# Kernel optimization log

Measured on AMD Instinct MI355X. Metric: run time of the kernel, lower is better.

Reference implementation:

```python
import jax, jax.numpy as jnp
import numpy as np

# dims
B, L, HID = 4, 4096, 1024
H, D = 16, 64            # num_mem_heads, head_dim = HID // H
DM = 128                 # mem_intermediate = head_dim * mem_expansion_factor (2.0)
K = 4                    # conv_kernel
CS = 64                  # chunk_size
EPS = 1e-6


def setup_inputs() -> dict:
    key = jax.random.key(0)
    ks = jax.random.split(key, 16)
    std = 0.02
    f = lambda i, shape: jax.random.normal(ks[i], shape, jnp.float32) * std
    return {
        'hidden_states': jax.random.normal(ks[0], (B, L, HID), jnp.float32),
        'Wq': f(1, (HID, HID)), 'Wk': f(2, (HID, HID)), 'Wv': f(3, (HID, HID)),
        'conv_q_w': f(4, (HID, K)), 'conv_q_b': jnp.zeros((HID,), jnp.float32),
        'conv_k_w': f(5, (HID, K)), 'conv_k_b': jnp.zeros((HID,), jnp.float32),
        'conv_v_w': f(6, (HID, K)), 'conv_v_b': jnp.zeros((HID,), jnp.float32),
        'q_norm_w': jnp.ones((D,), jnp.float32), 'k_norm_w': jnp.ones((D,), jnp.float32),
        'mem_decay_w': f(7, (H, HID)), 'mem_decay_b': jnp.zeros((H,), jnp.float32),
        'surprise_w': f(8, (H, HID)), 'surprise_b': jnp.zeros((H,), jnp.float32),
        'lr_w': f(9, (H, HID)), 'lr_b': jnp.zeros((H,), jnp.float32),
        'W1': f(10, (H, D, DM)), 'W2': f(11, (H, DM, D)),
    }


def _silu_bwd(x):
    sig = jax.nn.sigmoid(x)
    return sig + jax.nn.silu(x) * (1.0 - sig)


def _rmsnorm(x, w):
    xf = x.astype(jnp.float32)
    var = jnp.mean(xf * xf, axis=-1, keepdims=True)
    return w * (xf * jax.lax.rsqrt(var + EPS)).astype(x.dtype)


def _causal_conv_silu(x, w, b):
    # x: [B, L, H, D] -> depthwise causal conv over time on C=H*D channels -> [B, H, L, D]
    Bs, Ls, Hh, Dd = x.shape
    xc = jnp.swapaxes(x.reshape(Bs, Ls, Hh * Dd), 1, 2)        # [B, C, L]
    xp = jnp.pad(xc, ((0, 0), (0, 0), (K - 1, 0)))             # left pad -> causal
    y = b[None, :, None]
    for k in range(K):
        y = y + w[None, :, k:k + 1] * xp[:, :, k:k + Ls]
    y = jax.nn.silu(y)
    return jnp.swapaxes(y.reshape(Bs, Hh, Dd, Ls), -2, -1)     # [B, H, L, D]


def _decayed_scan(d, v, init):
    # y_t = d_t * y_{t-1} + v_t, y_0 = init; d: [B,H,C,1], v: [B,H,C,dim], init: [B,H,1,dim]
    def comb(x, y):
        a1, b1 = x
        a2, b2 = y
        return a1 * a2, b1 * a2 + b2
    A, Bv = jax.lax.associative_scan(comb, (d, v), axis=2)
    return A * init + Bv


def _forward(hidden_states, Wq, Wk, Wv, conv_q_w, conv_q_b, conv_k_w, conv_k_b,
             conv_v_w, conv_v_b, q_norm_w, k_norm_w, mem_decay_w, mem_decay_b,
             surprise_w, surprise_b, lr_w, lr_b, W1, W2):
    x = hidden_states
    # projections -> [B, L, H, D]
    q = (x @ Wq.T).reshape(B, L, H, D)
    k = (x @ Wk.T).reshape(B, L, H, D)
    v = (x @ Wv.T).reshape(B, L, H, D)
    # depthwise causal conv + silu -> [B, H, L, D]
    q = _causal_conv_silu(q, conv_q_w, conv_q_b)
    k = _causal_conv_silu(k, conv_k_w, conv_k_b)
    v = _causal_conv_silu(v, conv_v_w, conv_v_b)
    # QK RMSNorm (per head_dim)
    q = _rmsnorm(q, q_norm_w)
    k = _rmsnorm(k, k_norm_w)
    # per-timestep gates -> [B, H, L, 1]
    mem_decay = 1.0 - jax.nn.sigmoid(x @ mem_decay_w.T + mem_decay_b)
    surprise_decay = jax.nn.sigmoid(x @ surprise_w.T + surprise_b)
    lr = jax.nn.sigmoid(x @ lr_w.T + lr_b)
    to_gate = lambda g: jnp.swapaxes(g, -2, -1)[..., None]
    mem_decay, surprise_decay, lr = to_gate(mem_decay), to_gate(surprise_decay), to_gate(lr)

    # split sequence into chunks: [N, B, H, CS, *]
    N = L // CS
    ch = lambda t: jnp.moveaxis(t.reshape(B, H, N, CS, t.shape[-1]), 2, 0)
    qs, ks_, vs = ch(q), ch(k), ch(v)
    mds, sds, lrs = ch(mem_decay), ch(surprise_decay), ch(lr)

    W1b = jnp.broadcast_to(W1[None], (B, H, D, DM))
    W2b = jnp.broadcast_to(W2[None], (B, H, DM, D))
    carry0 = (W1b, W2b,
              jnp.zeros((B, H, 1, DM), jnp.float32),   # W1_surprise
              jnp.zeros((B, H, 1, D), jnp.float32),    # W2_surprise
              jnp.zeros((B, H, 1, D), jnp.float32),    # key_momentum
              jnp.zeros((B, H, 1, DM), jnp.float32))   # X1_momentum

    def step(carry, inp):
        W1c, W2c, W1s, W2s, kmom, xmom = carry
        qc, kc, vc, md, sd, lrc = inp
        # memory MLP fwd with chunk-frozen weights
        Z1 = kc @ W1c                       # [B,H,CS,DM]
        X1 = jax.nn.silu(Z1)
        mems = X1 @ W2c                     # [B,H,CS,D]
        g_m = mems - vc
        g_Z1 = (g_m @ jnp.swapaxes(W2c, -2, -1)) * _silu_bwd(Z1)
        g_m = -lrc * g_m
        g_Z1 = -lrc * g_Z1
        # activation-space surprise/momentum scans (decayed linear recurrence)
        W1s_n = _decayed_scan(sd, g_Z1, W1s)[:, :, -1:, :]
        W2s_n = _decayed_scan(sd, g_m, W2s)[:, :, -1:, :]
        kmom_n = _decayed_scan(md, kc, kmom)[:, :, -1:, :]
        xmom_n = _decayed_scan(md, X1, xmom)[:, :, -1:, :]
        # weight update at chunk boundary: decay + outer-product of accumulated factors
        mprod = jnp.prod(md, axis=2, keepdims=True)          # [B,H,1,1]
        W1n = mprod * W1c + jnp.swapaxes(kmom_n, -2, -1) @ W1s_n
        W2n = mprod * W2c + jnp.swapaxes(xmom_n, -2, -1) @ W2s_n
        # retrieve with updated memory
        y = jax.nn.silu(qc @ W1n) @ W2n                      # [B,H,CS,D]
        return (W1n, W2n, W1s_n, W2s_n, kmom_n, xmom_n), y

    _, ys = jax.lax.scan(step, carry0, (qs, ks_, vs, mds, sds, lrs))
    mem_states = jnp.moveaxis(ys, 0, 2).reshape(B, H, L, D)
    # replicate torch: mem_states.transpose(-2,-1).reshape(B, L, H*D)
    return jnp.swapaxes(mem_states, -2, -1).reshape(B, L, H * D)


def reference(hidden_states, Wq, Wk, Wv, conv_q_w, conv_q_b, conv_k_w, conv_k_b,
              conv_v_w, conv_v_b, q_norm_w, k_norm_w, mem_decay_w, mem_decay_b,
              surprise_w, surprise_b, lr_w, lr_b, W1, W2):
    return _forward(hidden_states, Wq, Wk, Wv, conv_q_w, conv_q_b, conv_k_w, conv_k_b,
                    conv_v_w, conv_v_b, q_norm_w, k_norm_w, mem_decay_w, mem_decay_b,
                    surprise_w, surprise_b, lr_w, lr_b, W1, W2)
```

## Files before the change

### kernel.cpp

```cpp
#include <hip/hip_runtime.h>

#define B_ 4
#define L_ 4096
#define HID_ 1024
#define H_ 16
#define D_ 64
#define DM_ 128
#define CS_ 64
#define NCH_ 64
#define EPS_ 1e-6f

typedef __attribute__((ext_vector_type(8))) short bfrag_t;
typedef __attribute__((ext_vector_type(4))) float facc_t;

#define MFMA16(a,b,c) __builtin_amdgcn_mfma_f32_16x16x32_bf16(a,b,c,0,0,0)

__device__ __forceinline__ float sigf(float x){ return 1.0f/(1.0f + __expf(-x)); }

__device__ __forceinline__ unsigned f2bfu(float x){
  unsigned u = __float_as_uint(x);
  return (u + 0x7fffu + ((u>>16)&1u)) >> 16;
}
__device__ __forceinline__ float bf2f(unsigned short s){
  return __uint_as_float(((unsigned)s)<<16);
}
__device__ __forceinline__ unsigned cvtpk(float lo, float hi){
  unsigned r;
  asm("v_cvt_pk_bf16_f32 %0, %1, %2" : "=v"(r) : "v"(lo), "v"(hi));
  return r;
}
__device__ __forceinline__ float bflo(unsigned u){ return __uint_as_float(u<<16); }
__device__ __forceinline__ float bfhi(unsigned u){ return __uint_as_float(u & 0xffff0000u); }

__device__ __forceinline__ void gld16(const unsigned short* g, unsigned short* l){
  __builtin_amdgcn_global_load_lds(
      (const __attribute__((address_space(1))) unsigned int*)(const void*)g,
      (__attribute__((address_space(3))) unsigned int*)(void*)l,
      16, 0, 0);
}

#define DPP_ADD_(x, ctrl) x += __int_as_float(__builtin_amdgcn_update_dpp(0, __float_as_int(x), ctrl, 0xf, 0xf, true))
__device__ __forceinline__ float wsum64(float x){
  DPP_ADD_(x, 0x111);
  DPP_ADD_(x, 0x112);
  DPP_ADD_(x, 0x114);
  DPP_ADD_(x, 0x118);
  const float a = __int_as_float(__builtin_amdgcn_readlane(__float_as_int(x), 15));
  const float b = __int_as_float(__builtin_amdgcn_readlane(__float_as_int(x), 31));
  const float c = __int_as_float(__builtin_amdgcn_readlane(__float_as_int(x), 47));
  const float d = __int_as_float(__builtin_amdgcn_readlane(__float_as_int(x), 63));
  return (a+b)+(c+d);
}

__global__ __launch_bounds__(256) void cast_kernel(
    const float* __restrict__ x,  const float* __restrict__ wq,
    const float* __restrict__ wk, const float* __restrict__ wv,
    unsigned short* __restrict__ xb,  unsigned short* __restrict__ wqb,
    unsigned short* __restrict__ wkb, unsigned short* __restrict__ wvb)
{
  const int bid = blockIdx.x;
  const float* s; unsigned short* d; int base;
  if (bid < 16384){ s = x; d = xb; base = bid*1024; }
  else {
    int r = bid - 16384; const int a = r >> 10; r &= 1023; base = r*1024;
    s = (a==0)?wq:(a==1)?wk:wv;
    d = (a==0)?wqb:(a==1)?wkb:wvb;
  }
  const int i = base + threadIdx.x*4;
  float4 v = *(const float4*)(s + i);
  unsigned lo = f2bfu(v.x) | (f2bfu(v.y)<<16);
  unsigned hi = f2bfu(v.z) | (f2bfu(v.w)<<16);
  uint2 o; o.x = lo; o.y = hi;
  *(uint2*)(d + i) = o;
}

__global__ __launch_bounds__(256, 2) void gemm_bf16_nt(
    const unsigned short* __restrict__ A, const unsigned short* __restrict__ Bw,
    unsigned short* __restrict__ C, int M, int N, int K)
{
  __shared__ __align__(16) unsigned short As[2][4096];
  __shared__ __align__(16) unsigned short Bs[2][4096];
  const int tid = threadIdx.x;
  const int lane = tid & 63, wave = tid >> 6;
  const int lq = lane & 15, quad = lane >> 4;
  const int m0 = blockIdx.y*128, n0 = blockIdx.x*128;
  const int row = tid >> 2, ks = (tid & 3)*8;
  const int mo = (wave & 1)*64, no = (wave >> 1)*64;

  const unsigned short* pa0 = A  + (size_t)(m0 + row)*K + ks;
  const unsigned short* pa1 = pa0 + (size_t)64*K;
  const unsigned short* pb0 = Bw + (size_t)(n0 + row)*K + ks;
  const unsigned short* pb1 = pb0 + (size_t)64*K;

  facc_t acc[4][4];
  #pragma unroll
  for (int i=0;i<4;++i)
    #pragma unroll
    for (int j=0;j<4;++j) acc[i][j] = (facc_t){0.f,0.f,0.f,0.f};

  auto stage = [&](int buf, int kt){
    const int off = kt*32;
    unsigned short* ab = &As[buf][wave*512];
    unsigned short* bb = &Bs[buf][wave*512];
    gld16(pa0 + off, ab);
    gld16(pa1 + off, ab + 2048);
    gld16(pb0 + off, bb);
    gld16(pb1 + off, bb + 2048);
  };

  const int kiters = K >> 5;
  stage(0, 0);
  __syncthreads();

  int cur = 0;
  for (int kt = 0; kt < kiters; ++kt){
    if (kt+1 < kiters) stage(cur^1, kt+1);
    bfrag_t af[4], bf[4];
    #pragma unroll
    for (int mt=0;mt<4;++mt) af[mt] = *(const bfrag_t*)&As[cur][(mo+mt*16+lq)*32 + quad*8];
    #pragma unroll
    for (int nt=0;nt<4;++nt) bf[nt] = *(const bfrag_t*)&Bs[cur][(no+nt*16+lq)*32 + quad*8];
    #pragma unroll
    for (int mt=0;mt<4;++mt)
      #pragma unroll
      for (int nt=0;nt<4;++nt)
        acc[mt][nt] = MFMA16(af[mt], bf[nt], acc[mt][nt]);
    __syncthreads();
    cur ^= 1;
  }

  #pragma unroll
  for (int mt=0;mt<4;++mt)
    #pragma unroll
    for (int nt=0;nt<4;++nt)
      #pragma unroll
      for (int r=0;r<4;++r){
        const int rr = m0 + mo + mt*16 + quad*4 + r;
        const int cc = n0 + no + nt*16 + lq;
        const int t = cc >> 10, hh = (cc >> 6) & 15, dd = cc & 63;
        const int b = rr >> 12, l = rr & 4095;
        C[((((size_t)t*B_ + b)*H_ + hh)*L_ + l)*64 + dd]
            = (unsigned short)f2bfu(acc[mt][nt][r]);
      }
}

__global__ __launch_bounds__(256, 2) void gates_kernel(
  const float* __restrict__ x,
  const float* __restrict__ mdw, const float* __restrict__ mdb,
  const float* __restrict__ sw,  const float* __restrict__ sb,
  const float* __restrict__ lw,  const float* __restrict__ lb,
  float* __restrict__ cmb, float* __restrict__ c1b, float* __restrict__ ppb)
{
  __shared__ float xs[64][68];
  __shared__ float wg[48][68];
  const int tid = threadIdx.x;
  const int m0 = blockIdx.x * 64;
  const int tx = tid & 15, ty = tid >> 4;
  float acc[4][3];
  #pragma unroll
  for (int r=0;r<4;++r){ acc[r][0]=0.f; acc[r][1]=0.f; acc[r][2]=0.f; }

  for (int k0 = 0; k0 < HID_; k0 += 64){
    {
      const int r = tid >> 2, kq = tid & 3;
      const float* xp = x + (size_t)(m0 + r) * HID_ + k0 + kq*16;
      #pragma unroll
      for (int u=0;u<4;++u){
        float4 v = *(const float4*)(xp + u*4);
        *(float4*)&xs[r][kq*16 + u*4] = v;
      }
    }
    #pragma unroll
    for (int u=0;u<3;++u){
      const int idx = tid + 256*u;
      const int gi = idx >> 4, q = idx & 15;
      const float* wp = (gi < 16) ? (mdw + (size_t)gi*HID_)
                      : (gi < 32) ? (sw  + (size_t)(gi-16)*HID_)
                                  : (lw  + (size_t)(gi-32)*HID_);
      float4 v = *(const float4*)(wp + k0 + q*4);
      *(float4*)&wg[gi][q*4] = v;
    }
    __syncthreads();
    for (int kk=0; kk<64; ++kk){
      float xv[4], wv[3];
      #pragma unroll
      for (int r=0;r<4;++r) xv[r] = xs[ty*4+r][kk];
      #pragma unroll
      for (int gg=0;gg<3;++gg) wv[gg] = wg[tx*3+gg][kk];
      #pragma unroll
      for (int r=0;r<4;++r)
        #pragma unroll
        for (int gg=0;gg<3;++gg) acc[r][gg] += xv[r]*wv[gg];
    }
    __syncthreads();
  }

  float (*ls)[68] = xs;
  #pragma unroll
  for (int gg=0; gg<3; ++gg){
    const int gi = tx*3 + gg;
    const int s = gi >> 4, hh = gi & 15;
    const float bias = (s==0) ? mdb[hh] : (s==1) ? sb[hh] : lb[hh];
    #pragma unroll
    for (int r=0;r<4;++r) ls[gi][ty*4+r] = acc[r][gg] + bias;
  }
  __syncthreads();

  const int lane = tid & 63, wv2 = tid >> 6;
  const int b = m0 >> 12, n = (m0 & 4095) >> 6;
  #pragma unroll
  for (int u=0;u<4;++u){
    const int hh = wv2*4 + u;
    const float md = 1.0f - sigf(ls[hh][lane]);
    const float sd = sigf(ls[16+hh][lane]);
    const float lr = sigf(ls[32+hh][lane]);
    float vm = md, vs = sd;
    #pragma unroll
    for (int off = 1; off < 64; off <<= 1){
      float om = __shfl_down(vm, off);
      float os = __shfl_down(vs, off);
      if (lane + off < 64){ vm *= om; vs *= os; }
    }
    float mex = __shfl_down(vm, 1);
    float sex = __shfl_down(vs, 1);
    if (lane == 63){ mex = 1.0f; sex = 1.0f; }
    const size_t base = ((size_t)(b*16 + hh)*NCH_ + n)*64;
    cmb[base + lane] = mex;
    c1b[base + lane] = -lr * sex;
    if (lane == 0){
      ppb[((size_t)(b*16+hh)*NCH_ + n)*2 + 0] = vm;
      ppb[((size_t)(b*16+hh)*NCH_ + n)*2 + 1] = vs;
    }
  }
}

#define HALO_T_ ((size_t)64*64*3*64)

__global__ __launch_bounds__(192) void halo_kernel(
  const unsigned short* __restrict__ qg, const unsigned short* __restrict__ kg,
  const unsigned short* __restrict__ vg, unsigned short* __restrict__ halo)
{
  const int blk = blockIdx.x;
  const int bh = blk / 63;
  const int ch = blk % 63 + 1;
  const int tid = threadIdx.x;
  const int tt = tid >> 6, lane = tid & 63;
  const long src = ((long)bh*L_ + (long)ch*64 - 3 + tt)*64 + lane;
  const long dst = (((long)bh*64 + ch)*3 + tt)*64 + lane;
  halo[dst]               = qg[src];
  halo[dst +   HALO_T_]   = kg[src];
  halo[dst + 2*HALO_T_]   = vg[src];
}

__global__ __launch_bounds__(256) void prep_kernel(
  unsigned short* __restrict__ qg, unsigned short* __restrict__ kg,
  unsigned short* __restrict__ vg,
  const unsigned short* __restrict__ halo,
  const float* __restrict__ cmg,
  const float* __restrict__ cqw, const float* __restrict__ cqb,
  const float* __restrict__ ckw, const float* __restrict__ ckb,
  const float* __restrict__ cvw, const float* __restrict__ cvb,
  const float* __restrict__ qnw, const float* __restrict__ knw,
  float* __restrict__ kredg)
{
  const int blk = blockIdx.x;
  const int bh = blk >> 6, ch = blk & 63;
  const int tid = threadIdx.x;
  const int lane = tid & 63, wave = tid >> 6;
  const int h = bh & 15;
  const int c = h*64 + lane;

  float wq4[4], wk4[4], wv4[4];
  #pragma unroll
  for (int kk=0;kk<4;++kk){ wq4[kk]=cqw[c*4+kk]; wk4[kk]=ckw[c*4+kk]; wv4[kk]=cvw[c*4+kk]; }
  const float bq = cqb[c], bk = ckb[c], bv = cvb[c];
  const float qnf = qnw[lane], knf = knw[lane];

  const long base = ((long)bh*L_ + (long)ch*64)*64 + lane;
  const int r0 = wave*16;

  float qw_[3], kw_[3], vw_[3];
  #pragma unroll
  for (int t=0;t<3;++t){
    const int row = r0 - 3 + t;
    if (row >= 0){
      qw_[t] = bf2f(qg[base + (long)row*64]);
      kw_[t] = bf2f(kg[base + (long)row*64]);
      vw_[t] = bf2f(vg[base + (long)row*64]);
    } else if (ch == 0){
      qw_[t] = 0.f; kw_[t] = 0.f; vw_[t] = 0.f;
    } else {
      const long hb = (((long)bh*64 + ch)*3 + (row + 3))*64 + lane;
      qw_[t] = bf2f(halo[hb]);
      kw_[t] = bf2f(halo[hb +   HALO_T_]);
      vw_[t] = bf2f(halo[hb + 2*HALO_T_]);
    }
  }
  __syncthreads();

  const float* cmp = cmg + ((size_t)bh*NCH_ + ch)*64;
  float kp = 0.f;
  #pragma unroll 8
  for (int i=0;i<16;++i){
    const int row = r0 + i;
    const long a = base + (long)row*64;
    const float q0v = bf2f(qg[a]);
    const float k0v = bf2f(kg[a]);
    const float v0v = bf2f(vg[a]);
    float aq = bq + wq4[0]*qw_[0] + wq4[1]*qw_[1] + wq4[2]*qw_[2] + wq4[3]*q0v;
    float ak = bk + wk4[0]*kw_[0] + wk4[1]*kw_[1] + wk4[2]*kw_[2] + wk4[3]*k0v;
    float av = bv + wv4[0]*vw_[0] + wv4[1]*vw_[1] + wv4[2]*vw_[2] + wv4[3]*v0v;
    const float yk = ak*sigf(ak), yq = aq*sigf(aq), yv = av*sigf(av);
    const float ssk = wsum64(yk*yk);
    const float ssq = wsum64(yq*yq);
    const float vk = knf * yk * rsqrtf(ssk*(1.0f/64.0f) + EPS_);
    const float vq = qnf * yq * rsqrtf(ssq*(1.0f/64.0f) + EPS_);
    const unsigned short kb16 = (unsigned short)f2bfu(vk);
    qg[a] = (unsigned short)f2bfu(vq);
    kg[a] = kb16;
    vg[a] = (unsigned short)f2bfu(yv);
    kp += cmp[row] * bf2f(kb16);
    qw_[0]=qw_[1]; qw_[1]=qw_[2]; qw_[2]=q0v;
    kw_[0]=kw_[1]; kw_[1]=kw_[2]; kw_[2]=k0v;
    vw_[0]=vw_[1]; vw_[1]=vw_[2]; vw_[2]=v0v;
  }

  __shared__ float kpart[4][64];
  kpart[wave][lane] = kp;
  __syncthreads();
  if (wave == 0)
    kredg[((size_t)bh*NCH_ + ch)*64 + lane] =
        (kpart[0][lane]+kpart[1][lane]) + (kpart[2][lane]+kpart[3][lane]);
}

#define SK 72
#define SX 136

__global__ __launch_bounds__(1024, 4) void scan_kernel(
  const unsigned short* __restrict__ qg, const unsigned short* __restrict__ kg,
  const unsigned short* __restrict__ vg,
  const float* __restrict__ cmg, const float* __restrict__ c1g,
  const float* __restrict__ ppg, const float* __restrict__ krg,
  const float* __restrict__ W1in, const float* __restrict__ W2in,
  float* __restrict__ out)
{
  const int bh = blockIdx.x;
  const int h = bh & 15;
  const int tid = threadIdx.x;
  const int lane = tid & 63, wave = tid >> 6;
  const int lq = lane & 15, quad = lane >> 4;
  const int wg = wave & 3;
  const int rw = wg * 16;
  const int cw = wave >> 2;

  __shared__ __align__(16) unsigned short sm[63488];
  unsigned short* xbs = sm + 27648;
  unsigned short* W1T = sm + 36352;
  unsigned short* W2n = sm + 45568;
  unsigned short* W2T = sm + 54784;
  __shared__ float cmA[2][64], c1A[2][64], krA[2][64], ppS[2][2];
  __shared__ float kmomS[64], xmomS[128], w1momS[128], w2momS[64];
  __shared__ float xpart[4][128], w1part[4][128], w2part[4][64];

  {
    const int j = tid >> 3, q0 = (tid & 7) * 8;
    const float* w1p = W1in + (size_t)h * D_ * DM_;
    #pragma unroll
    for (int t=0;t<8;++t)
      W1T[j*SK + q0 + t] = (unsigned short)f2bfu(w1p[(size_t)(q0+t)*DM_ + j]);
    const float* w2p = W2in + (size_t)h * DM_ * D_ + (size_t)j*D_ + q0;
    #pragma unroll
    for (int t=0;t<8;++t){
      unsigned short v = (unsigned short)f2bfu(w2p[t]);
      W2n[j*SK + q0 + t] = v;
      W2T[(q0+t)*SX + j] = v;
    }
  }
  if (tid < 64){ kmomS[tid]=0.f; w2momS[tid]=0.f; }
  if (tid < 128){ xmomS[tid]=0.f; w1momS[tid]=0.f; }

  const long cbase = (long)bh * L_ * 64;
  const int tr = tid >> 4, tc = (tid & 15) * 4;

  uint2 rq2, rk2, rv2;
  float cmr=0.f, c1r=0.f, krr=0.f, ppr=0.f;

  auto stage_load = [&](int m){
    if (m >= NCH_) return;
    const long a = cbase + ((long)m*64 + tr)*64 + tc;
    rq2 = *(const uint2*)(qg + a);
    rk2 = *(const uint2*)(kg + a);
    rv2 = *(const uint2*)(vg + a);
    if (wave == 0){
      cmr = cmg[((size_t)bh*NCH_ + m)*64 + lane];
      c1r = c1g[((size_t)bh*NCH_ + m)*64 + lane];
      krr = krg[((size_t)bh*NCH_ + m)*64 + lane];
    }
    if (tid < 2) ppr = ppg[((size_t)bh*NCH_ + m)*2 + tid];
  };

  auto stage_store = [&](int m, int s){
    if (m >= NCH_) return;
    unsigned short* kc = sm + s*4608;
    unsigned short* qc = sm + 9216 + s*4608;
    unsigned short* gm = sm + 18432 + s*4608;
    *(uint2*)&kc[tr*SK + tc] = rk2;
    *(uint2*)&qc[tr*SK + tc] = rq2;
    *(uint2*)&gm[tr*SK + tc] = rv2;
    if (wave == 0){ cmA[s][lane] = cmr; c1A[s][lane] = c1r; krA[s][lane] = krr; }
    if (tid < 2) ppS[s][tid] = ppr;
  };

  stage_load(0);
  stage_store(0, 0);
  __syncthreads();

  for (int n = 0; n < NCH_; ++n){
    const int cur = n & 1, nxt = cur ^ 1;
    const unsigned short* kcs = sm + cur*4608;
    const unsigned short* qcs = sm + 9216 + cur*4608;
    unsigned short* gms = sm + 18432 + cur*4608;
    const int r0 = rw + quad*4;

    stage_load(n+1);

    facc_t zk[2];
    {
      const bfrag_t a0 = *(const bfrag_t*)&kcs[(rw+lq)*SK + quad*8];
      const bfrag_t a1 = *(const bfrag_t*)&kcs[(rw+lq)*SK + 32 + quad*8];
      const float4 cmv = *(const float4*)&cmA[cur][r0];
      #pragma unroll
      for (int nt=0;nt<2;++nt){
        const int j = cw*32 + nt*16 + lq;
        const bfrag_t b0 = *(const bfrag_t*)&W1T[j*SK + quad*8];
        const bfrag_t b1 = *(const bfrag_t*)&W1T[j*SK + 32 + quad*8];
        facc_t z = {0.f,0.f,0.f,0.f};
        z = MFMA16(a0,b0,z); z = MFMA16(a1,b1,z);
        zk[nt] = z;
        const float x0 = z[0]*sigf(z[0]), x1 = z[1]*sigf(z[1]);
        const float x2 = z[2]*sigf(z[2]), x3 = z[3]*sigf(z[3]);
        const unsigned p01 = cvtpk(x0,x1), p23 = cvtpk(x2,x3);
        xbs[(r0+0)*SX + j] = (unsigned short)p01;
        xbs[(r0+1)*SX + j] = (unsigned short)(p01>>16);
        xbs[(r0+2)*SX + j] = (unsigned short)p23;
        xbs[(r0+3)*SX + j] = (unsigned short)(p23>>16);
        float xp = cmv.x*x0 + cmv.y*x1 + cmv.z*x2 + cmv.w*x3;
        xp += __shfl_xor(xp, 16);
        xp += __shfl_xor(xp, 32);
        if (quad == 0) xpart[wg][j] = xp;
      }
    }
    __syncthreads();

    {
      bfrag_t xa[4];
      #pragma unroll
      for (int kt=0;kt<4;++kt) xa[kt] = *(const bfrag_t*)&xbs[(rw+lq)*SX + kt*32 + quad*8];
      const int e = cw*16 + lq;
      facc_t z = {0.f,0.f,0.f,0.f};
      #pragma unroll
      for (int kt=0;kt<4;++kt){
        const bfrag_t bb = *(const bfrag_t*)&W2T[e*SX + kt*32 + quad*8];
        z = MFMA16(xa[kt], bb, z);
      }
      const float g0 = z[0] - bf2f(gms[(r0+0)*SK + e]);
      const float g1 = z[1] - bf2f(gms[(r0+1)*SK + e]);
      const float g2 = z[2] - bf2f(gms[(r0+2)*SK + e]);
      const float g3 = z[3] - bf2f(gms[(r0+3)*SK + e]);
      const unsigned p01 = cvtpk(g0,g1), p23 = cvtpk(g2,g3);
      gms[(r0+0)*SK + e] = (unsigned short)p01;
      gms[(r0+1)*SK + e] = (unsigned short)(p01>>16);
      gms[(r0+2)*SK + e] = (unsigned short)p23;
      gms[(r0+3)*SK + e] = (unsigned short)(p23>>16);
      const float4 c1v = *(const float4*)&c1A[cur][r0];
      float wp = c1v.x*g0 + c1v.y*g1 + c1v.z*g2 + c1v.w*g3;
      wp += __shfl_xor(wp, 16);
      wp += __shfl_xor(wp, 32);
      if (quad == 0) w2part[wg][e] = wp;
    }
    if (tid < 64) kmomS[tid] = ppS[cur][0]*kmomS[tid] + krA[cur][tid];
    if (tid < 128)
      xmomS[tid] = ppS[cur][0]*xmomS[tid]
                 + ((xpart[0][tid]+xpart[1][tid])+(xpart[2][tid]+xpart[3][tid]));
    stage_store(n+1, nxt);
    __syncthreads();

    {
      const bfrag_t a0 = *(const bfrag_t*)&gms[(rw+lq)*SK + quad*8];
      const bfrag_t a1 = *(const bfrag_t*)&gms[(rw+lq)*SK + 32 + quad*8];
      const float4 c1v = *(const float4*)&c1A[cur][r0];
      #pragma unroll
      for (int nt=0;nt<2;++nt){
        const int j = cw*32 + nt*16 + lq;
        const bfrag_t b0 = *(const bfrag_t*)&W2n[j*SK + quad*8];
        const bfrag_t b1 = *(const bfrag_t*)&W2n[j*SK + 32 + quad*8];
        facc_t gz = {0.f,0.f,0.f,0.f};
        gz = MFMA16(a0,b0,gz); gz = MFMA16(a1,b1,gz);
        float d[4];
        #pragma unroll
        for (int r=0;r<4;++r){
          const float zz = zk[nt][r];
          const float sg = sigf(zz);
          d[r] = gz[r] * (sg * (1.0f + zz*(1.0f - sg)));
        }
        const unsigned p01 = cvtpk(d[0],d[1]), p23 = cvtpk(d[2],d[3]);
        xbs[(r0+0)*SX + j] = (unsigned short)p01;
        xbs[(r0+1)*SX + j] = (unsigned short)(p01>>16);
        xbs[(r0+2)*SX + j] = (unsigned short)p23;
        xbs[(r0+3)*SX + j] = (unsigned short)(p23>>16);
        float wp = c1v.x*d[0] + c1v.y*d[1] + c1v.z*d[2] + c1v.w*d[3];
        wp += __shfl_xor(wp, 16);
        wp += __shfl_xor(wp, 32);
        if (quad == 0) w1part[wg][j] = wp;
      }
    }
    if (tid < 64)
      w2momS[tid] = ppS[cur][1]*w2momS[tid]
                  + ((w2part[0][tid]+w2part[1][tid])+(w2part[2][tid]+w2part[3][tid]));
    __syncthreads();

    {
      const float Pmd = ppS[cur][0], Psd = ppS[cur][1];
      const int j = tid >> 3, q0 = (tid & 7)*8;
      const float w1m = Psd*w1momS[j]
          + ((w1part[0][j]+w1part[1][j])+(w1part[2][j]+w1part[3][j]));
      if ((tid & 7) == 0) w1momS[j] = w1m;
      const float xm = xmomS[j];
      const float4 km0 = *(const float4*)&kmomS[q0];
      const float4 km1 = *(const float4*)&kmomS[q0+4];
      {
        const int off = j*SK + q0;
        const uint4 w = *(const uint4*)&W1T[off];
        uint4 o;
        o.x = cvtpk(Pmd*bflo(w.x) + w1m*km0.x, Pmd*bfhi(w.x) + w1m*km0.y);
        o.y = cvtpk(Pmd*bflo(w.y) + w1m*km0.z, Pmd*bfhi(w.y) + w1m*km0.w);
        o.z = cvtpk(Pmd*bflo(w.z) + w1m*km1.x, Pmd*bfhi(w.z) + w1m*km1.y);
        o.w = cvtpk(Pmd*bflo(w.w) + w1m*km1.z, Pmd*bfhi(w.w) + w1m*km1.w);
        *(uint4*)&W1T[off] = o;
      }
      const float4 wm0 = *(const float4*)&w2momS[q0];
      const float4 wm1 = *(const float4*)&w2momS[q0+4];
      {
        const int off = j*SK + q0;
        const uint4 w = *(const uint4*)&W2n[off];
        uint4 o;
        o.x = cvtpk(Pmd*bflo(w.x) + xm*wm0.x, Pmd*bfhi(w.x) + xm*wm0.y);
        o.y = cvtpk(Pmd*bflo(w.y) + xm*wm0.z, Pmd*bfhi(w.y) + xm*wm0.w);
        o.z = cvtpk(Pmd*bflo(w.z) + xm*wm1.x, Pmd*bfhi(w.z) + xm*wm1.y);
        o.w = cvtpk(Pmd*bflo(w.w) + xm*wm1.z, Pmd*bfhi(w.w) + xm*wm1.w);
        *(uint4*)&W2n[off] = o;
      }
      const int e2 = tid >> 4, js = (tid & 15)*8;
      const float w2m = w2momS[e2];
      const float4 xm0 = *(const float4*)&xmomS[js];
      const float4 xm1 = *(const float4*)&xmomS[js+4];
      {
        const int off = e2*SX + js;
        const uint4 w = *(const uint4*)&W2T[off];
        uint4 o;
        o.x = cvtpk(Pmd*bflo(w.x) + xm0.x*w2m, Pmd*bfhi(w.x) + xm0.y*w2m);
        o.y = cvtpk(Pmd*bflo(w.y) + xm0.z*w2m, Pmd*bfhi(w.y) + xm0.w*w2m);
        o.z = cvtpk(Pmd*bflo(w.z) + xm1.x*w2m, Pmd*bfhi(w.z) + xm1.y*w2m);
        o.w = cvtpk(Pmd*bflo(w.w) + xm1.z*w2m, Pmd*bfhi(w.w) + xm1.w*w2m);
        *(uint4*)&W2T[off] = o;
      }
    }
    __syncthreads();

    {
      const bfrag_t a0 = *(const bfrag_t*)&qcs[(rw+lq)*SK + quad*8];
      const bfrag_t a1 = *(const bfrag_t*)&qcs[(rw+lq)*SK + 32 + quad*8];
      #pragma unroll
      for (int nt=0;nt<2;++nt){
        const int j = cw*32 + nt*16 + lq;
        const bfrag_t b0 = *(const bfrag_t*)&W1T[j*SK + quad*8];
        const bfrag_t b1 = *(const bfrag_t*)&W1T[j*SK + 32 + quad*8];
        facc_t z = {0.f,0.f,0.f,0.f};
        z = MFMA16(a0,b0,z); z = MFMA16(a1,b1,z);
        const float x0 = z[0]*sigf(z[0]), x1 = z[1]*sigf(z[1]);
        const float x2 = z[2]*sigf(z[2]), x3 = z[3]*sigf(z[3]);
        const unsigned p01 = cvtpk(x0,x1), p23 = cvtpk(x2,x3);
        xbs[(r0+0)*SX + j] = (unsigned short)p01;
        xbs[(r0+1)*SX + j] = (unsigned short)(p01>>16);
        xbs[(r0+2)*SX + j] = (unsigned short)p23;
        xbs[(r0+3)*SX + j] = (unsigned short)(p23>>16);
      }
    }
    __syncthreads();

    {
      bfrag_t xa[4];
      #pragma unroll
      for (int kt=0;kt<4;++kt) xa[kt] = *(const bfrag_t*)&xbs[(rw+lq)*SX + kt*32 + quad*8];
      const int e = cw*16 + lq;
      facc_t y = {0.f,0.f,0.f,0.f};
      #pragma unroll
      for (int kt=0;kt<4;++kt){
        const bfrag_t bb = *(const bfrag_t*)&W2T[e*SX + kt*32 + quad*8];
        y = MFMA16(xa[kt], bb, y);
      }
      float4 ov; ov.x = y[0]; ov.y = y[1]; ov.z = y[2]; ov.w = y[3];
      *(float4*)&out[(size_t)bh*D_*L_ + (size_t)e*L_ + n*64 + rw + quad*4] = ov;
    }
    __syncthreads();
  }
}

extern "C" void kernel_launch(void* const* d_in, const int* in_sizes, int n_in,
                              void* d_out, int out_size, void* d_ws, size_t ws_size,
                              hipStream_t stream)
{
  const float* x   = (const float*)d_in[0];
  const float* Wq  = (const float*)d_in[1];
  const float* Wk  = (const float*)d_in[2];
  const float* Wv  = (const float*)d_in[3];
  const float* cqw = (const float*)d_in[4];
  const float* cqb = (const float*)d_in[5];
  const float* ckw = (const float*)d_in[6];
  const float* ckb = (const float*)d_in[7];
  const float* cvw = (const float*)d_in[8];
  const float* cvb = (const float*)d_in[9];
  const float* qnw = (const float*)d_in[10];
  const float* knw = (const float*)d_in[11];
  const float* mdw = (const float*)d_in[12];
  const float* mdb = (const float*)d_in[13];
  const float* sw  = (const float*)d_in[14];
  const float* sb  = (const float*)d_in[15];
  const float* lw  = (const float*)d_in[16];
  const float* lb  = (const float*)d_in[17];
  const float* W1  = (const float*)d_in[18];
  const float* W2  = (const float*)d_in[19];
  float* out = (float*)d_out;

  const size_t SZ  = (size_t)B_ * L_ * HID_;
  const size_t WSZ = (size_t)HID_ * HID_;
  unsigned short* xb  = (unsigned short*)d_ws;
  unsigned short* wqb = xb  + SZ;
  unsigned short* wkb = wqb + WSZ;
  unsigned short* wvb = wkb + WSZ;
  unsigned short* qb  = wvb + WSZ;
  unsigned short* kb  = qb  + SZ;
  unsigned short* vb  = kb  + SZ;
  float* cmb = (float*)(vb + SZ);
  float* c1b = cmb + (size_t)B_*H_*NCH_*64;
  float* ppb = c1b + (size_t)B_*H_*NCH_*64;
  float* kredg = ppb + (size_t)B_*H_*NCH_*2;
  unsigned short* halo = (unsigned short*)(kredg + (size_t)B_*H_*NCH_*64);

  cast_kernel<<<16384 + 3*1024, 256, 0, stream>>>(x, Wq, Wk, Wv, xb, wqb, wkb, wvb);
  dim3 gg(3*HID_/128, (B_*L_)/128);
  gemm_bf16_nt<<<gg, 256, 0, stream>>>(xb, wqb, qb, B_*L_, 3*HID_, HID_);
  gates_kernel<<<(B_*L_)/64, 256, 0, stream>>>(x, mdw, mdb, sw, sb, lw, lb, cmb, c1b, ppb);
  halo_kernel<<<64*63, 192, 0, stream>>>(qb, kb, vb, halo);
  prep_kernel<<<B_*H_*NCH_, 256, 0, stream>>>(qb, kb, vb, halo, cmb,
                                              cqw, cqb, ckw, ckb, cvw, cvb,
                                              qnw, knw, kredg);
  scan_kernel<<<B_*H_, 1024, 0, stream>>>(qb, kb, vb, cmb, c1b, ppb, kredg,
                                          W1, W2, out);
}
```

Baseline: 772.6 us.

## Pipeline next-chunk key projection into scan retrieval and vectorize GEMM epilogue

The scan kernel now runs the next chunk's key-projection phase right after the query retrieval. It uses a separate LDS buffer for the retrieval activations and moves the staging store, which removes one barrier per chunk. The bf16 GEMM swaps its MFMA operands so each lane holds consecutive columns and can write packed 8-byte stores instead of scalar shorts. The cast kernel uses packed conversion, and the gates kernel reads LDS as float4. The gate buffers also reuse the start of the workspace, aliasing the bf16 input copy that is dead after the GEMM. LDS use in the scan kernel grows, which may limit occupancy.

After: 797.5 us. 1.03x slower.

```diff
diff --git a/kernel.cpp b/kernel.cpp
--- a/kernel.cpp
+++ b/kernel.cpp
@@ -68,8 +68,8 @@
   }
   const int i = base + threadIdx.x*4;
   float4 v = *(const float4*)(s + i);
-  unsigned lo = f2bfu(v.x) | (f2bfu(v.y)<<16);
-  unsigned hi = f2bfu(v.z) | (f2bfu(v.w)<<16);
+  unsigned lo = cvtpk(v.x, v.y);
+  unsigned hi = cvtpk(v.z, v.w);
   uint2 o; o.x = lo; o.y = hi;
   *(uint2*)(d + i) = o;
 }
@@ -124,7 +124,7 @@
     for (int mt=0;mt<4;++mt)
       #pragma unroll
       for (int nt=0;nt<4;++nt)
-        acc[mt][nt] = MFMA16(af[mt], bf[nt], acc[mt][nt]);
+        acc[mt][nt] = MFMA16(bf[nt], af[mt], acc[mt][nt]);
     __syncthreads();
     cur ^= 1;
   }
@@ -132,16 +132,16 @@
   #pragma unroll
   for (int mt=0;mt<4;++mt)
     #pragma unroll
-    for (int nt=0;nt<4;++nt)
-      #pragma unroll
-      for (int r=0;r<4;++r){
-        const int rr = m0 + mo + mt*16 + quad*4 + r;
-        const int cc = n0 + no + nt*16 + lq;
-        const int t = cc >> 10, hh = (cc >> 6) & 15, dd = cc & 63;
-        const int b = rr >> 12, l = rr & 4095;
-        C[((((size_t)t*B_ + b)*H_ + hh)*L_ + l)*64 + dd]
-            = (unsigned short)f2bfu(acc[mt][nt][r]);
-      }
+    for (int nt=0;nt<4;++nt){
+      const int rr  = m0 + mo + mt*16 + lq;
+      const int cc0 = n0 + no + nt*16 + quad*4;
+      const int t = cc0 >> 10, hh = (cc0 >> 6) & 15, dd0 = cc0 & 63;
+      const int b = rr >> 12, l = rr & 4095;
+      uint2 ov;
+      ov.x = cvtpk(acc[mt][nt][0], acc[mt][nt][1]);
+      ov.y = cvtpk(acc[mt][nt][2], acc[mt][nt][3]);
+      *(uint2*)&C[((((size_t)t*B_ + b)*H_ + hh)*L_ + l)*64 + dd0] = ov;
+    }
 }
 
 __global__ __launch_bounds__(256, 2) void gates_kernel(
@@ -181,16 +181,18 @@
       *(float4*)&wg[gi][q*4] = v;
     }
     __syncthreads();
-    for (int kk=0; kk<64; ++kk){
-      float xv[4], wv[3];
-      #pragma unroll
-      for (int r=0;r<4;++r) xv[r] = xs[ty*4+r][kk];
-      #pragma unroll
-      for (int gg=0;gg<3;++gg) wv[gg] = wg[tx*3+gg][kk];
-      #pragma unroll
-      for (int r=0;r<4;++r)
+    #pragma unroll 4
+    for (int kk=0; kk<64; kk+=4){
+      float4 wv[3];
+      #pragma unroll
+      for (int gg=0;gg<3;++gg) wv[gg] = *(const float4*)&wg[tx*3+gg][kk];
+      #pragma unroll
+      for (int r=0;r<4;++r){
+        const float4 xv = *(const float4*)&xs[ty*4+r][kk];
         #pragma unroll
-        for (int gg=0;gg<3;++gg) acc[r][gg] += xv[r]*wv[gg];
+        for (int gg=0;gg<3;++gg)
+          acc[r][gg] += xv.x*wv[gg].x + xv.y*wv[gg].y + xv.z*wv[gg].z + xv.w*wv[gg].w;
+      }
     }
     __syncthreads();
   }
@@ -352,12 +354,14 @@
   const int wg = wave & 3;
   const int rw = wg * 16;
   const int cw = wave >> 2;
-
-  __shared__ __align__(16) unsigned short sm[63488];
-  unsigned short* xbs = sm + 27648;
-  unsigned short* W1T = sm + 36352;
-  unsigned short* W2n = sm + 45568;
-  unsigned short* W2T = sm + 54784;
+  const int r0 = rw + quad*4;
+
+  __shared__ __align__(16) unsigned short sm[72192];
+  unsigned short* xbuf = sm + 27648;
+  unsigned short* hqb  = sm + 36352;
+  unsigned short* W1T  = sm + 45056;
+  unsigned short* W2n  = sm + 54272;
+  unsigned short* W2T  = sm + 63488;
   __shared__ float cmA[2][64], c1A[2][64], krA[2][64], ppS[2][2];
   __shared__ float kmomS[64], xmomS[128], w1momS[128], w2momS[64];
   __shared__ float xpart[4][128], w1part[4][128], w2part[4][64];
@@ -411,51 +415,52 @@
     if (tid < 2) ppS[s][tid] = ppr;
   };
 
+  facc_t zk[2];
+
+  auto phaseP2 = [&](int s){
+    const unsigned short* kcs = sm + s*4608;
+    const bfrag_t a0 = *(const bfrag_t*)&kcs[(rw+lq)*SK + quad*8];
+    const bfrag_t a1 = *(const bfrag_t*)&kcs[(rw+lq)*SK + 32 + quad*8];
+    const float4 cmv = *(const float4*)&cmA[s][r0];
+    #pragma unroll
+    for (int nt=0;nt<2;++nt){
+      const int j = cw*32 + nt*16 + lq;
+      const bfrag_t b0 = *(const bfrag_t*)&W1T[j*SK + quad*8];
+      const bfrag_t b1 = *(const bfrag_t*)&W1T[j*SK + 32 + quad*8];
+      facc_t z = {0.f,0.f,0.f,0.f};
+      z = MFMA16(a0,b0,z); z = MFMA16(a1,b1,z);
+      zk[nt] = z;
+      const float x0 = z[0]*sigf(z[0]), x1 = z[1]*sigf(z[1]);
+      const float x2 = z[2]*sigf(z[2]), x3 = z[3]*sigf(z[3]);
+      const unsigned p01 = cvtpk(x0,x1), p23 = cvtpk(x2,x3);
+      xbuf[(r0+0)*SX + j] = (unsigned short)p01;
+      xbuf[(r0+1)*SX + j] = (unsigned short)(p01>>16);
+      xbuf[(r0+2)*SX + j] = (unsigned short)p23;
+      xbuf[(r0+3)*SX + j] = (unsigned short)(p23>>16);
+      float xp = cmv.x*x0 + cmv.y*x1 + cmv.z*x2 + cmv.w*x3;
+      xp += __shfl_xor(xp, 16);
+      xp += __shfl_xor(xp, 32);
+      if (quad == 0) xpart[wg][j] = xp;
+    }
+  };
+
   stage_load(0);
   stage_store(0, 0);
   __syncthreads();
+  phaseP2(0);
+  __syncthreads();
 
   for (int n = 0; n < NCH_; ++n){
     const int cur = n & 1, nxt = cur ^ 1;
-    const unsigned short* kcs = sm + cur*4608;
     const unsigned short* qcs = sm + 9216 + cur*4608;
     unsigned short* gms = sm + 18432 + cur*4608;
-    const int r0 = rw + quad*4;
 
     stage_load(n+1);
-
-    facc_t zk[2];
-    {
-      const bfrag_t a0 = *(const bfrag_t*)&kcs[(rw+lq)*SK + quad*8];
-      const bfrag_t a1 = *(const bfrag_t*)&kcs[(rw+lq)*SK + 32 + quad*8];
-      const float4 cmv = *(const float4*)&cmA[cur][r0];
-      #pragma unroll
-      for (int nt=0;nt<2;++nt){
-        const int j = cw*32 + nt*16 + lq;
-        const bfrag_t b0 = *(const bfrag_t*)&W1T[j*SK + quad*8];
-        const bfrag_t b1 = *(const bfrag_t*)&W1T[j*SK + 32 + quad*8];
-        facc_t z = {0.f,0.f,0.f,0.f};
-        z = MFMA16(a0,b0,z); z = MFMA16(a1,b1,z);
-        zk[nt] = z;
-        const float x0 = z[0]*sigf(z[0]), x1 = z[1]*sigf(z[1]);
-        const float x2 = z[2]*sigf(z[2]), x3 = z[3]*sigf(z[3]);
-        const unsigned p01 = cvtpk(x0,x1), p23 = cvtpk(x2,x3);
-        xbs[(r0+0)*SX + j] = (unsigned short)p01;
-        xbs[(r0+1)*SX + j] = (unsigned short)(p01>>16);
-        xbs[(r0+2)*SX + j] = (unsigned short)p23;
-        xbs[(r0+3)*SX + j] = (unsigned short)(p23>>16);
-        float xp = cmv.x*x0 + cmv.y*x1 + cmv.z*x2 + cmv.w*x3;
-        xp += __shfl_xor(xp, 16);
-        xp += __shfl_xor(xp, 32);
-        if (quad == 0) xpart[wg][j] = xp;
-      }
-    }
-    __syncthreads();
 
     {
       bfrag_t xa[4];
       #pragma unroll
-      for (int kt=0;kt<4;++kt) xa[kt] = *(const bfrag_t*)&xbs[(rw+lq)*SX + kt*32 + quad*8];
+      for (int kt=0;kt<4;++kt) xa[kt] = *(const bfrag_t*)&xbuf[(rw+lq)*SX + kt*32 + quad*8];
       const int e = cw*16 + lq;
       facc_t z = {0.f,0.f,0.f,0.f};
       #pragma unroll
@@ -482,7 +487,6 @@
     if (tid < 128)
       xmomS[tid] = ppS[cur][0]*xmomS[tid]
                  + ((xpart[0][tid]+xpart[1][tid])+(xpart[2][tid]+xpart[3][tid]));
-    stage_store(n+1, nxt);
     __syncthreads();
 
     {
@@ -504,10 +508,10 @@
           d[r] = gz[r] * (sg * (1.0f + zz*(1.0f - sg)));
         }
         const unsigned p01 = cvtpk(d[0],d[1]), p23 = cvtpk(d[2],d[3]);
-        xbs[(r0+0)*SX + j] = (unsigned short)p01;
-        xbs[(r0+1)*SX + j] = (unsigned short)(p01>>16);
-        xbs[(r0+2)*SX + j] = (unsigned short)p23;
-        xbs[(r0+3)*SX + j] = (unsigned short)(p23>>16);
+        xbuf[(r0+0)*SX + j] = (unsigned short)p01;
+        xbuf[(r0+1)*SX + j] = (unsigned short)(p01>>16);
+        xbuf[(r0+2)*SX + j] = (unsigned short)p23;
+        xbuf[(r0+3)*SX + j] = (unsigned short)(p23>>16);
         float wp = c1v.x*d[0] + c1v.y*d[1] + c1v.z*d[2] + c1v.w*d[3];
         wp += __shfl_xor(wp, 16);
         wp += __shfl_xor(wp, 32);
@@ -517,6 +521,7 @@
     if (tid < 64)
       w2momS[tid] = ppS[cur][1]*w2momS[tid]
                   + ((w2part[0][tid]+w2part[1][tid])+(w2part[2][tid]+w2part[3][tid]));
+    stage_store(n+1, nxt);
     __syncthreads();
 
     {
@@ -572,26 +577,24 @@
       const bfrag_t a1 = *(const bfrag_t*)&qcs[(rw+lq)*SK + 32 + quad*8];
       #pragma unroll
       for (int nt=0;nt<2;++nt){
-        const int j = cw*32 + nt*16 + lq;
-        const bfrag_t b0 = *(const bfrag_t*)&W1T[j*SK + quad*8];
-        const bfrag_t b1 = *(const bfrag_t*)&W1T[j*SK + 32 + quad*8];
+        const int j0 = cw*32 + nt*16;
+        const bfrag_t b0 = *(const bfrag_t*)&W1T[(j0+lq)*SK + quad*8];
+        const bfrag_t b1 = *(const bfrag_t*)&W1T[(j0+lq)*SK + 32 + quad*8];
         facc_t z = {0.f,0.f,0.f,0.f};
-        z = MFMA16(a0,b0,z); z = MFMA16(a1,b1,z);
+        z = MFMA16(b0,a0,z); z = MFMA16(b1,a1,z);
         const float x0 = z[0]*sigf(z[0]), x1 = z[1]*sigf(z[1]);
         const float x2 = z[2]*sigf(z[2]), x3 = z[3]*sigf(z[3]);
-        const unsigned p01 = cvtpk(x0,x1), p23 = cvtpk(x2,x3);
-        xbs[(r0+0)*SX + j] = (unsigned short)p01;
-        xbs[(r0+1)*SX + j] = (unsigned short)(p01>>16);
-        xbs[(r0+2)*SX + j] = (unsigned short)p23;
-        xbs[(r0+3)*SX + j] = (unsigned short)(p23>>16);
-      }
-    }
-    __syncthreads();
-
+        uint2 o; o.x = cvtpk(x0,x1); o.y = cvtpk(x2,x3);
+        *(uint2*)&hqb[(rw+lq)*SX + j0 + quad*4] = o;
+      }
+    }
+    __syncthreads();
+
+    if (n+1 < NCH_) phaseP2(nxt);
     {
       bfrag_t xa[4];
       #pragma unroll
-      for (int kt=0;kt<4;++kt) xa[kt] = *(const bfrag_t*)&xbs[(rw+lq)*SX + kt*32 + quad*8];
+      for (int kt=0;kt<4;++kt) xa[kt] = *(const bfrag_t*)&hqb[(rw+lq)*SX + kt*32 + quad*8];
       const int e = cw*16 + lq;
       facc_t y = {0.f,0.f,0.f,0.f};
       #pragma unroll
@@ -641,7 +644,7 @@
   unsigned short* qb  = wvb + WSZ;
   unsigned short* kb  = qb  + SZ;
   unsigned short* vb  = kb  + SZ;
-  float* cmb = (float*)(vb + SZ);
+  float* cmb = (float*)d_ws;
   float* c1b = cmb + (size_t)B_*H_*NCH_*64;
   float* ppb = c1b + (size_t)B_*H_*NCH_*64;
   float* kredg = ppb + (size_t)B_*H_*NCH_*2;
```
